# Kernel tuning notes

Hardware: AMD Instinct MI355X
Metric: run time of the kernel (lower is better)

Reference implementation:

```python
import jax, jax.numpy as jnp
import numpy as np

N = 262144  # number of points / sequence length
D = 64      # feature dim (qkv_dim); deterministic features => nb_features == D
KERNEL_EPSILON = 1e-3


def setup_inputs() -> dict:
    key = jax.random.key(0)
    ks = jax.random.split(key, 7)
    s = 1.0 / np.sqrt(D)
    return {
        "x": jax.random.normal(ks[0], (N, D), dtype=jnp.float32),
        "Wq": jax.random.normal(ks[1], (D, D), dtype=jnp.float32) * s,
        "bq": jnp.zeros((D,), dtype=jnp.float32),
        "Wk": jax.random.normal(ks[2], (D, D), dtype=jnp.float32) * s,
        "bk": jnp.zeros((D,), dtype=jnp.float32),
        "Wv": jax.random.normal(ks[3], (D, D), dtype=jnp.float32) * s,
        "bv": jnp.zeros((D,), dtype=jnp.float32),
    }


def reference(x, Wq, bq, Wk, bk, Wv, bv):
    # Dense projections (flax nn.Dense: x @ W + b)
    q = x @ Wq + bq  # [N, D]
    k = x @ Wk + bk
    v = x @ Wv + bv
    # Deterministic generalized kernel feature map: relu(data) + kernel_epsilon
    qp = jax.nn.relu(q) + KERNEL_EPSILON  # [N, M], M == D
    kp = jax.nn.relu(k) + KERNEL_EPSILON  # [N, M]
    # Bidirectional FAVOR+ linear attention: O(N*M*D)
    kv = jnp.einsum("nm,nd->md", kp, v)       # [M, D]
    num = jnp.einsum("nm,md->nd", qp, kv)     # [N, D]
    # renormalize_attention=True: divide by qp . sum(kp)
    denom = qp @ kp.sum(axis=0)               # [N]
    return num / denom[:, None]
```

## Files before the change

kernel.cpp:

```cpp
#include <hip/hip_runtime.h>
#include <hip/hip_bf16.h>


#define NPTS 262144
#define TILES (NPTS / 64)
#define GRID1 512
#define TPB1 (TILES / GRID1)
#define GRID2 1024
#define TPB2 (TILES / GRID2)
#define EPS 1e-3f

typedef __attribute__((ext_vector_type(8))) short short8;
typedef __attribute__((ext_vector_type(4))) float f32x4;

__device__ __forceinline__ unsigned short f2bf(float f) {
    unsigned u = __builtin_bit_cast(unsigned, f);
    u += 0x7FFFu + ((u >> 16) & 1u);
    return (unsigned short)(u >> 16);
}

__device__ __forceinline__ short8 load_bfrag(const float* __restrict__ W, int kk, int lg, int col) {
    short8 t;
    const float* p = W + (size_t)(kk * 32 + lg * 8) * 64 + col;
#pragma unroll
    for (int e = 0; e < 8; ++e) t[e] = (short)f2bf(p[(size_t)e * 64]);
    return t;
}

__device__ __forceinline__ short8 cvt8(float4 p0, float4 p1) {
    short8 a;
    a[0] = (short)f2bf(p0.x); a[1] = (short)f2bf(p0.y); a[2] = (short)f2bf(p0.z); a[3] = (short)f2bf(p0.w);
    a[4] = (short)f2bf(p1.x); a[5] = (short)f2bf(p1.y); a[6] = (short)f2bf(p1.z); a[7] = (short)f2bf(p1.w);
    return a;
}

__device__ __forceinline__ void lds_barrier() {
    asm volatile("s_waitcnt lgkmcnt(0)" ::: "memory");
    __builtin_amdgcn_s_barrier();
}

__global__ __launch_bounds__(256, 2) void pass1_kernel(
    const float* __restrict__ x, const float* __restrict__ Wk, const float* __restrict__ bk,
    const float* __restrict__ Wv, const float* __restrict__ bv,
    float* __restrict__ kvPart, float* __restrict__ ksPart)
{
    __shared__ unsigned short kpT[64][72];
    __shared__ unsigned short vT[64][72];
    __shared__ unsigned short wkF[8][64][8];
    __shared__ unsigned short wvF[8][64][8];

    const int tid = threadIdx.x;
    const int w = tid >> 6, l = tid & 63, l15 = l & 15, lg = l >> 4;

    {
        const float* W = (w < 2) ? Wk : Wv;
        int jbase = (w & 1) * 2;
#pragma unroll
        for (int jj = 0; jj < 2; ++jj)
#pragma unroll
            for (int kk = 0; kk < 2; ++kk) {
                short8 f = load_bfrag(W, kk, lg, (jbase + jj) * 16 + l15);
                if (w < 2) *(short8*)&wkF[(jbase + jj) * 2 + kk][l][0] = f;
                else       *(short8*)&wvF[(jbase + jj) * 2 + kk][l][0] = f;
            }
    }
    float bkl[4], bvl[4];
#pragma unroll
    for (int j = 0; j < 4; ++j) { bkl[j] = bk[j * 16 + l15]; bvl[j] = bv[j * 16 + l15]; }

    f32x4 akv[4];
#pragma unroll
    for (int j = 0; j < 4; ++j) akv[j] = (f32x4){0.f, 0.f, 0.f, 0.f};
    float ks[4] = {0.f, 0.f, 0.f, 0.f};

    lds_barrier();

    const int t0 = blockIdx.x * TPB1;
    const float* xbase = x + ((size_t)t0 * 64 + w * 16 + l15) * 64 + lg * 8;
    float4 c0 = *(const float4*)(xbase + 0);
    float4 c1 = *(const float4*)(xbase + 4);
    float4 c2 = *(const float4*)(xbase + 32);
    float4 c3 = *(const float4*)(xbase + 36);

    for (int t = 0; t < TPB1; ++t) {
        const float* xn = xbase + (size_t)((t + 1 < TPB1) ? (t + 1) : t) * 4096;
        float4 n0 = *(const float4*)(xn + 0);
        float4 n1 = *(const float4*)(xn + 4);
        float4 n2 = *(const float4*)(xn + 32);
        float4 n3 = *(const float4*)(xn + 36);

        short8 a0 = cvt8(c0, c1);
        short8 a1 = cvt8(c2, c3);

        const int nbase = w * 16 + lg * 4;
#pragma unroll
        for (int j = 0; j < 4; ++j) {
            short8 bk0 = *(const short8*)&wkF[j * 2 + 0][l][0];
            short8 bk1 = *(const short8*)&wkF[j * 2 + 1][l][0];
            short8 bv0 = *(const short8*)&wvF[j * 2 + 0][l][0];
            short8 bv1 = *(const short8*)&wvF[j * 2 + 1][l][0];
            f32x4 z = (f32x4){0.f, 0.f, 0.f, 0.f};
            f32x4 ak = __builtin_amdgcn_mfma_f32_16x16x32_bf16(a0, bk0, z, 0, 0, 0);
            ak = __builtin_amdgcn_mfma_f32_16x16x32_bf16(a1, bk1, ak, 0, 0, 0);
            f32x4 av = __builtin_amdgcn_mfma_f32_16x16x32_bf16(a0, bv0, z, 0, 0, 0);
            av = __builtin_amdgcn_mfma_f32_16x16x32_bf16(a1, bv1, av, 0, 0, 0);
            unsigned short h[4], g[4];
#pragma unroll
            for (int r = 0; r < 4; ++r) {
                float kp = fmaxf(ak[r] + bkl[j], 0.f) + EPS;
                ks[j] += kp;
                h[r] = f2bf(kp);
                g[r] = f2bf(av[r] + bvl[j]);
            }
            uint2 hp, gp;
            hp.x = (unsigned)h[0] | ((unsigned)h[1] << 16);
            hp.y = (unsigned)h[2] | ((unsigned)h[3] << 16);
            gp.x = (unsigned)g[0] | ((unsigned)g[1] << 16);
            gp.y = (unsigned)g[2] | ((unsigned)g[3] << 16);
            *(uint2*)&kpT[j * 16 + l15][nbase] = hp;
            *(uint2*)&vT[j * 16 + l15][nbase] = gp;
        }
        lds_barrier();
        short8 ka0 = *(const short8*)&kpT[w * 16 + l15][lg * 8];
        short8 ka1 = *(const short8*)&kpT[w * 16 + l15][32 + lg * 8];
#pragma unroll
        for (int j = 0; j < 4; ++j) {
            short8 vb0 = *(const short8*)&vT[j * 16 + l15][lg * 8];
            short8 vb1 = *(const short8*)&vT[j * 16 + l15][32 + lg * 8];
            akv[j] = __builtin_amdgcn_mfma_f32_16x16x32_bf16(ka0, vb0, akv[j], 0, 0, 0);
            akv[j] = __builtin_amdgcn_mfma_f32_16x16x32_bf16(ka1, vb1, akv[j], 0, 0, 0);
        }
        lds_barrier();
        c0 = n0; c1 = n1; c2 = n2; c3 = n3;
    }

    float* kvs = kvPart + (size_t)blockIdx.x * 4096;
#pragma unroll
    for (int j = 0; j < 4; ++j)
#pragma unroll
        for (int r = 0; r < 4; ++r)
            kvs[(size_t)(w * 16 + lg * 4 + r) * 64 + j * 16 + l15] = akv[j][r];
#pragma unroll
    for (int j = 0; j < 4; ++j) {
        float s = ks[j];
        s += __shfl_xor(s, 16, 64);
        s += __shfl_xor(s, 32, 64);
        if (lg == 0) ksPart[(size_t)blockIdx.x * 256 + w * 64 + j * 16 + l15] = s;
    }
}

__global__ __launch_bounds__(256, 4) void reduce_kernel(
    const float* __restrict__ kvPart, const float* __restrict__ ksPart,
    float* __restrict__ kvFin, float* __restrict__ ksFin)
{
    __shared__ float red[4][64];
    const int b = blockIdx.x, t = threadIdx.x;
    const int oo = t & 63, sc = t >> 6;
    float acc = 0.f;
    if (b < 64) {
        const float* p = kvPart + (size_t)sc * 128 * 4096 + b * 64 + oo;
#pragma unroll 8
        for (int s = 0; s < GRID1 / 4; ++s) acc += p[(size_t)s * 4096];
    } else {
        const float* p = ksPart + (size_t)sc * (GRID1) * 64 + oo;
#pragma unroll 8
        for (int s = 0; s < GRID1; ++s) acc += p[(size_t)s * 64];
    }
    red[sc][oo] = acc;
    __syncthreads();
    if (t < 64) {
        float s = red[0][t] + red[1][t] + red[2][t] + red[3][t];
        if (b < 64) kvFin[b * 64 + t] = s;
        else        ksFin[t] = s;
    }
}

__global__ __launch_bounds__(256, 4) void pass2_kernel(
    const float* __restrict__ x, const float* __restrict__ Wq, const float* __restrict__ bq,
    const float* __restrict__ kvFin, const float* __restrict__ ksFin,
    float* __restrict__ out)
{
    __shared__ unsigned short qpL[64][72];
    __shared__ unsigned short wqF[8][64][8];
    __shared__ unsigned short kvF[8][64][8];

    const int tid = threadIdx.x;
    const int w = tid >> 6, l = tid & 63, l15 = l & 15, lg = l >> 4;

#pragma unroll
    for (int kk = 0; kk < 2; ++kk) {
        short8 f = load_bfrag(Wq, kk, lg, w * 16 + l15);
        *(short8*)&wqF[w * 2 + kk][l][0] = f;
        short8 g = load_bfrag(kvFin, kk, lg, w * 16 + l15);
        *(short8*)&kvF[w * 2 + kk][l][0] = g;
    }
    float bql[4], ksl[4];
#pragma unroll
    for (int j = 0; j < 4; ++j) { bql[j] = bq[j * 16 + l15]; ksl[j] = ksFin[j * 16 + l15]; }

    lds_barrier();

    const int t0 = blockIdx.x * TPB2;
    const float* xbase = x + ((size_t)t0 * 64 + w * 16 + l15) * 64 + lg * 8;
    float4 c0 = *(const float4*)(xbase + 0);
    float4 c1 = *(const float4*)(xbase + 4);
    float4 c2 = *(const float4*)(xbase + 32);
    float4 c3 = *(const float4*)(xbase + 36);

    for (int t = 0; t < TPB2; ++t) {
        const float* xn = xbase + (size_t)((t + 1 < TPB2) ? (t + 1) : t) * 4096;
        float4 n0 = *(const float4*)(xn + 0);
        float4 n1 = *(const float4*)(xn + 4);
        float4 n2 = *(const float4*)(xn + 32);
        float4 n3 = *(const float4*)(xn + 36);

        short8 a0 = cvt8(c0, c1);
        short8 a1 = cvt8(c2, c3);

        float qp[4][4];
#pragma unroll
        for (int j = 0; j < 4; ++j) {
            short8 bq0 = *(const short8*)&wqF[j * 2 + 0][l][0];
            short8 bq1 = *(const short8*)&wqF[j * 2 + 1][l][0];
            f32x4 z = (f32x4){0.f, 0.f, 0.f, 0.f};
            f32x4 aq = __builtin_amdgcn_mfma_f32_16x16x32_bf16(a0, bq0, z, 0, 0, 0);
            aq = __builtin_amdgcn_mfma_f32_16x16x32_bf16(a1, bq1, aq, 0, 0, 0);
#pragma unroll
            for (int r = 0; r < 4; ++r) qp[j][r] = fmaxf(aq[r] + bql[j], 0.f) + EPS;
        }
        float dp[4];
#pragma unroll
        for (int r = 0; r < 4; ++r)
            dp[r] = qp[0][r] * ksl[0] + qp[1][r] * ksl[1] + qp[2][r] * ksl[2] + qp[3][r] * ksl[3];
#pragma unroll
        for (int mask = 1; mask <= 8; mask <<= 1)
#pragma unroll
            for (int r = 0; r < 4; ++r) dp[r] += __shfl_xor(dp[r], mask, 64);

        const int nb = w * 16 + lg * 4;
#pragma unroll
        for (int j = 0; j < 4; ++j)
#pragma unroll
            for (int r = 0; r < 4; ++r)
                qpL[nb + r][j * 16 + l15] = f2bf(qp[j][r]);
        lds_barrier();

        short8 an0 = *(const short8*)&qpL[w * 16 + l15][lg * 8];
        short8 an1 = *(const short8*)&qpL[w * 16 + l15][32 + lg * 8];
        float inv[4];
#pragma unroll
        for (int r = 0; r < 4; ++r) inv[r] = __builtin_amdgcn_rcpf(dp[r]);
        const int row0 = (t0 + t) * 64 + w * 16;
#pragma unroll
        for (int j = 0; j < 4; ++j) {
            short8 kv0 = *(const short8*)&kvF[j * 2 + 0][l][0];
            short8 kv1 = *(const short8*)&kvF[j * 2 + 1][l][0];
            f32x4 z = (f32x4){0.f, 0.f, 0.f, 0.f};
            f32x4 nm = __builtin_amdgcn_mfma_f32_16x16x32_bf16(an0, kv0, z, 0, 0, 0);
            nm = __builtin_amdgcn_mfma_f32_16x16x32_bf16(an1, kv1, nm, 0, 0, 0);
#pragma unroll
            for (int r = 0; r < 4; ++r)
                out[(size_t)(row0 + lg * 4 + r) * 64 + j * 16 + l15] = nm[r] * inv[r];
        }
        lds_barrier();
        c0 = n0; c1 = n1; c2 = n2; c3 = n3;
    }
}

extern "C" void kernel_launch(void* const* d_in, const int* in_sizes, int n_in,
                              void* d_out, int out_size, void* d_ws, size_t ws_size,
                              hipStream_t stream)
{
    const float* x  = (const float*)d_in[0];
    const float* Wq = (const float*)d_in[1];
    const float* bq = (const float*)d_in[2];
    const float* Wk = (const float*)d_in[3];
    const float* bk = (const float*)d_in[4];
    const float* Wv = (const float*)d_in[5];
    const float* bv = (const float*)d_in[6];
    float* out = (float*)d_out;

    float* kvPart = (float*)d_ws;
    float* ksPart = kvPart + (size_t)GRID1 * 4096;
    float* kvFin  = ksPart + (size_t)GRID1 * 256;
    float* ksFin  = kvFin + 4096;

    hipLaunchKernelGGL(pass1_kernel, dim3(GRID1), dim3(256), 0, stream,
                       x, Wk, bk, Wv, bv, kvPart, ksPart);
    hipLaunchKernelGGL(reduce_kernel, dim3(65), dim3(256), 0, stream,
                       kvPart, ksPart, kvFin, ksFin);
    hipLaunchKernelGGL(pass2_kernel, dim3(GRID2), dim3(256), 0, stream,
                       x, Wq, bq, kvFin, ksFin, out);
}
```

Baseline: 61.69 us.

## Keep KV accumulation per-wave in registers and drop block barriers in both passes

In pass1, each wave now processes two 16-row tiles at once. The K and V fragments for 32 rows are packed directly into MFMA operands, so a full 64x64 KV accumulator lives per wave in registers. This removes the per-tile LDS transpose and its two block barriers. A tree reduction through LDS at the end combines the four waves' accumulators before writing the partials. In pass2, each wave only reads back its own rows of qp, so the block barriers are replaced by a wave-local lgkmcnt drain with a double-buffered LDS tile. The cost is a 64-float accumulator array per thread in pass1, which raises register pressure and may hurt occupancy or cause spills.

```diff
diff --git a/kernel.cpp b/kernel.cpp
--- a/kernel.cpp
+++ b/kernel.cpp
@@ -6,6 +6,7 @@
 #define TILES (NPTS / 64)
 #define GRID1 512
 #define TPB1 (TILES / GRID1)
+#define PAIRS1 (TPB1 / 2)
 #define GRID2 1024
 #define TPB2 (TILES / GRID2)
 #define EPS 1e-3f
@@ -38,16 +39,19 @@
     asm volatile("s_waitcnt lgkmcnt(0)" ::: "memory");
     __builtin_amdgcn_s_barrier();
 }
+__device__ __forceinline__ void lds_drain() {
+    asm volatile("s_waitcnt lgkmcnt(0)" ::: "memory");
+}
 
 __global__ __launch_bounds__(256, 2) void pass1_kernel(
     const float* __restrict__ x, const float* __restrict__ Wk, const float* __restrict__ bk,
     const float* __restrict__ Wv, const float* __restrict__ bv,
     float* __restrict__ kvPart, float* __restrict__ ksPart)
 {
-    __shared__ unsigned short kpT[64][72];
-    __shared__ unsigned short vT[64][72];
     __shared__ unsigned short wkF[8][64][8];
     __shared__ unsigned short wvF[8][64][8];
+    __shared__ float redA[4096];
+    __shared__ float redB[4096];
 
     const int tid = threadIdx.x;
     const int w = tid >> 6, l = tid & 63, l15 = l & 15, lg = l >> 4;
@@ -68,31 +72,42 @@
 #pragma unroll
     for (int j = 0; j < 4; ++j) { bkl[j] = bk[j * 16 + l15]; bvl[j] = bv[j * 16 + l15]; }
 
-    f32x4 akv[4];
-#pragma unroll
-    for (int j = 0; j < 4; ++j) akv[j] = (f32x4){0.f, 0.f, 0.f, 0.f};
+    f32x4 akv[4][4];
+#pragma unroll
+    for (int jm = 0; jm < 4; ++jm)
+#pragma unroll
+        for (int jd = 0; jd < 4; ++jd) akv[jm][jd] = (f32x4){0.f, 0.f, 0.f, 0.f};
     float ks[4] = {0.f, 0.f, 0.f, 0.f};
 
     lds_barrier();
 
     const int t0 = blockIdx.x * TPB1;
     const float* xbase = x + ((size_t)t0 * 64 + w * 16 + l15) * 64 + lg * 8;
-    float4 c0 = *(const float4*)(xbase + 0);
-    float4 c1 = *(const float4*)(xbase + 4);
-    float4 c2 = *(const float4*)(xbase + 32);
-    float4 c3 = *(const float4*)(xbase + 36);
-
-    for (int t = 0; t < TPB1; ++t) {
-        const float* xn = xbase + (size_t)((t + 1 < TPB1) ? (t + 1) : t) * 4096;
-        float4 n0 = *(const float4*)(xn + 0);
-        float4 n1 = *(const float4*)(xn + 4);
-        float4 n2 = *(const float4*)(xn + 32);
-        float4 n3 = *(const float4*)(xn + 36);
-
-        short8 a0 = cvt8(c0, c1);
-        short8 a1 = cvt8(c2, c3);
-
-        const int nbase = w * 16 + lg * 4;
+    float4 cA0 = *(const float4*)(xbase + 0);
+    float4 cA1 = *(const float4*)(xbase + 4);
+    float4 cA2 = *(const float4*)(xbase + 32);
+    float4 cA3 = *(const float4*)(xbase + 36);
+    float4 cB0 = *(const float4*)(xbase + 4096 + 0);
+    float4 cB1 = *(const float4*)(xbase + 4096 + 4);
+    float4 cB2 = *(const float4*)(xbase + 4096 + 32);
+    float4 cB3 = *(const float4*)(xbase + 4096 + 36);
+
+#pragma unroll
+    for (int p = 0; p < PAIRS1; ++p) {
+        const float* xn = xbase + (size_t)((p + 1 < PAIRS1) ? (p + 1) : p) * 8192;
+        float4 nA0 = *(const float4*)(xn + 0);
+        float4 nA1 = *(const float4*)(xn + 4);
+        float4 nA2 = *(const float4*)(xn + 32);
+        float4 nA3 = *(const float4*)(xn + 36);
+        float4 nB0 = *(const float4*)(xn + 4096 + 0);
+        float4 nB1 = *(const float4*)(xn + 4096 + 4);
+        float4 nB2 = *(const float4*)(xn + 4096 + 32);
+        float4 nB3 = *(const float4*)(xn + 4096 + 36);
+
+        short8 a0A = cvt8(cA0, cA1), a1A = cvt8(cA2, cA3);
+        short8 a0B = cvt8(cB0, cB1), a1B = cvt8(cB2, cB3);
+
+        short8 kpc[4], vc[4];
 #pragma unroll
         for (int j = 0; j < 4; ++j) {
             short8 bk0 = *(const short8*)&wkF[j * 2 + 0][l][0];
@@ -100,46 +115,78 @@
             short8 bv0 = *(const short8*)&wvF[j * 2 + 0][l][0];
             short8 bv1 = *(const short8*)&wvF[j * 2 + 1][l][0];
             f32x4 z = (f32x4){0.f, 0.f, 0.f, 0.f};
-            f32x4 ak = __builtin_amdgcn_mfma_f32_16x16x32_bf16(a0, bk0, z, 0, 0, 0);
-            ak = __builtin_amdgcn_mfma_f32_16x16x32_bf16(a1, bk1, ak, 0, 0, 0);
-            f32x4 av = __builtin_amdgcn_mfma_f32_16x16x32_bf16(a0, bv0, z, 0, 0, 0);
-            av = __builtin_amdgcn_mfma_f32_16x16x32_bf16(a1, bv1, av, 0, 0, 0);
-            unsigned short h[4], g[4];
+            f32x4 akA = __builtin_amdgcn_mfma_f32_16x16x32_bf16(a0A, bk0, z, 0, 0, 0);
+            akA = __builtin_amdgcn_mfma_f32_16x16x32_bf16(a1A, bk1, akA, 0, 0, 0);
+            f32x4 avA = __builtin_amdgcn_mfma_f32_16x16x32_bf16(a0A, bv0, z, 0, 0, 0);
+            avA = __builtin_amdgcn_mfma_f32_16x16x32_bf16(a1A, bv1, avA, 0, 0, 0);
+            f32x4 akB = __builtin_amdgcn_mfma_f32_16x16x32_bf16(a0B, bk0, z, 0, 0, 0);
+            akB = __builtin_amdgcn_mfma_f32_16x16x32_bf16(a1B, bk1, akB, 0, 0, 0);
+            f32x4 avB = __builtin_amdgcn_mfma_f32_16x16x32_bf16(a0B, bv0, z, 0, 0, 0);
+            avB = __builtin_amdgcn_mfma_f32_16x16x32_bf16(a1B, bv1, avB, 0, 0, 0);
+            short8 kc, vv;
 #pragma unroll
             for (int r = 0; r < 4; ++r) {
-                float kp = fmaxf(ak[r] + bkl[j], 0.f) + EPS;
-                ks[j] += kp;
-                h[r] = f2bf(kp);
-                g[r] = f2bf(av[r] + bvl[j]);
+                float kA = fmaxf(akA[r] + bkl[j], 0.f) + EPS;
+                float kB = fmaxf(akB[r] + bkl[j], 0.f) + EPS;
+                ks[j] += kA + kB;
+                kc[r] = (short)f2bf(kA);
+                kc[4 + r] = (short)f2bf(kB);
+                vv[r] = (short)f2bf(avA[r] + bvl[j]);
+                vv[4 + r] = (short)f2bf(avB[r] + bvl[j]);
             }
-            uint2 hp, gp;
-            hp.x = (unsigned)h[0] | ((unsigned)h[1] << 16);
-            hp.y = (unsigned)h[2] | ((unsigned)h[3] << 16);
-            gp.x = (unsigned)g[0] | ((unsigned)g[1] << 16);
-            gp.y = (unsigned)g[2] | ((unsigned)g[3] << 16);
-            *(uint2*)&kpT[j * 16 + l15][nbase] = hp;
-            *(uint2*)&vT[j * 16 + l15][nbase] = gp;
+            kpc[j] = kc; vc[j] = vv;
         }
-        lds_barrier();
-        short8 ka0 = *(const short8*)&kpT[w * 16 + l15][lg * 8];
-        short8 ka1 = *(const short8*)&kpT[w * 16 + l15][32 + lg * 8];
-#pragma unroll
-        for (int j = 0; j < 4; ++j) {
-            short8 vb0 = *(const short8*)&vT[j * 16 + l15][lg * 8];
-            short8 vb1 = *(const short8*)&vT[j * 16 + l15][32 + lg * 8];
-            akv[j] = __builtin_amdgcn_mfma_f32_16x16x32_bf16(ka0, vb0, akv[j], 0, 0, 0);
-            akv[j] = __builtin_amdgcn_mfma_f32_16x16x32_bf16(ka1, vb1, akv[j], 0, 0, 0);
-        }
-        lds_barrier();
-        c0 = n0; c1 = n1; c2 = n2; c3 = n3;
-    }
-
-    float* kvs = kvPart + (size_t)blockIdx.x * 4096;
-#pragma unroll
-    for (int j = 0; j < 4; ++j)
-#pragma unroll
-        for (int r = 0; r < 4; ++r)
-            kvs[(size_t)(w * 16 + lg * 4 + r) * 64 + j * 16 + l15] = akv[j][r];
+#pragma unroll
+        for (int jm = 0; jm < 4; ++jm)
+#pragma unroll
+            for (int jd = 0; jd < 4; ++jd)
+                akv[jm][jd] = __builtin_amdgcn_mfma_f32_16x16x32_bf16(kpc[jm], vc[jd], akv[jm][jd], 0, 0, 0);
+
+        cA0 = nA0; cA1 = nA1; cA2 = nA2; cA3 = nA3;
+        cB0 = nB0; cB1 = nB1; cB2 = nB2; cB3 = nB3;
+    }
+
+#define KV_IDX(jm, jd, r) ((size_t)((jm) * 16 + lg * 4 + (r)) * 64 + (jd) * 16 + l15)
+    if (w == 1 || w == 3) {
+        float* dst = (w == 1) ? redA : redB;
+#pragma unroll
+        for (int jm = 0; jm < 4; ++jm)
+#pragma unroll
+            for (int jd = 0; jd < 4; ++jd)
+#pragma unroll
+                for (int r = 0; r < 4; ++r) dst[KV_IDX(jm, jd, r)] = akv[jm][jd][r];
+    }
+    __syncthreads();
+    if (w == 0 || w == 2) {
+        const float* src = (w == 0) ? redA : redB;
+#pragma unroll
+        for (int jm = 0; jm < 4; ++jm)
+#pragma unroll
+            for (int jd = 0; jd < 4; ++jd)
+#pragma unroll
+                for (int r = 0; r < 4; ++r) akv[jm][jd][r] += src[KV_IDX(jm, jd, r)];
+    }
+    __syncthreads();
+    if (w == 2) {
+#pragma unroll
+        for (int jm = 0; jm < 4; ++jm)
+#pragma unroll
+            for (int jd = 0; jd < 4; ++jd)
+#pragma unroll
+                for (int r = 0; r < 4; ++r) redA[KV_IDX(jm, jd, r)] = akv[jm][jd][r];
+    }
+    __syncthreads();
+    if (w == 0) {
+        float* kvs = kvPart + (size_t)blockIdx.x * 4096;
+#pragma unroll
+        for (int jm = 0; jm < 4; ++jm)
+#pragma unroll
+            for (int jd = 0; jd < 4; ++jd)
+#pragma unroll
+                for (int r = 0; r < 4; ++r)
+                    kvs[KV_IDX(jm, jd, r)] = akv[jm][jd][r] + redA[KV_IDX(jm, jd, r)];
+    }
+#undef KV_IDX
 #pragma unroll
     for (int j = 0; j < 4; ++j) {
         float s = ks[j];
@@ -180,7 +227,7 @@
     const float* __restrict__ kvFin, const float* __restrict__ ksFin,
     float* __restrict__ out)
 {
-    __shared__ unsigned short qpL[64][72];
+    __shared__ unsigned short qpS[2][64][72];
     __shared__ unsigned short wqF[8][64][8];
     __shared__ unsigned short kvF[8][64][8];
 
@@ -207,6 +254,7 @@
     float4 c2 = *(const float4*)(xbase + 32);
     float4 c3 = *(const float4*)(xbase + 36);
 
+#pragma unroll
     for (int t = 0; t < TPB2; ++t) {
         const float* xn = xbase + (size_t)((t + 1 < TPB2) ? (t + 1) : t) * 4096;
         float4 n0 = *(const float4*)(xn + 0);
@@ -237,16 +285,17 @@
 #pragma unroll
             for (int r = 0; r < 4; ++r) dp[r] += __shfl_xor(dp[r], mask, 64);
 
+        const int buf = t & 1;
         const int nb = w * 16 + lg * 4;
 #pragma unroll
         for (int j = 0; j < 4; ++j)
 #pragma unroll
             for (int r = 0; r < 4; ++r)
-                qpL[nb + r][j * 16 + l15] = f2bf(qp[j][r]);
-        lds_barrier();
-
-        short8 an0 = *(const short8*)&qpL[w * 16 + l15][lg * 8];
-        short8 an1 = *(const short8*)&qpL[w * 16 + l15][32 + lg * 8];
+                qpS[buf][nb + r][j * 16 + l15] = f2bf(qp[j][r]);
+        lds_drain();
+
+        short8 an0 = *(const short8*)&qpS[buf][w * 16 + l15][lg * 8];
+        short8 an1 = *(const short8*)&qpS[buf][w * 16 + l15][32 + lg * 8];
         float inv[4];
 #pragma unroll
         for (int r = 0; r < 4; ++r) inv[r] = __builtin_amdgcn_rcpf(dp[r]);
@@ -262,7 +311,6 @@
             for (int r = 0; r < 4; ++r)
                 out[(size_t)(row0 + lg * 4 + r) * 64 + j * 16 + l15] = nm[r] * inv[r];
         }
-        lds_barrier();
         c0 = n0; c1 = n1; c2 = n2; c3 = n3;
     }
 }
```

After: 67.37 us. +9.2%, slower.

## Compute Q features in pass1, store bf16 qp to workspace for pass2

Applied to the files above, without the earlier changes.

Moves the Q projection and ReLU feature map into the first pass, writing qp as bf16 to workspace so the second pass reads half-size qp instead of re-reading x in fp32 and recomputing. The denominator is computed with an MFMA against bf16-rounded key sums, and weight staging now uses coalesced row loads transposed through LDS. This trades extra workspace writes and heavier pass1 work for a lighter pass2, with roughly unchanged total DRAM bytes and slightly lower denominator precision.

```diff
diff --git a/kernel.cpp b/kernel.cpp
--- a/kernel.cpp
+++ b/kernel.cpp
@@ -19,14 +19,6 @@
     return (unsigned short)(u >> 16);
 }
 
-__device__ __forceinline__ short8 load_bfrag(const float* __restrict__ W, int kk, int lg, int col) {
-    short8 t;
-    const float* p = W + (size_t)(kk * 32 + lg * 8) * 64 + col;
-#pragma unroll
-    for (int e = 0; e < 8; ++e) t[e] = (short)f2bf(p[(size_t)e * 64]);
-    return t;
-}
-
 __device__ __forceinline__ short8 cvt8(float4 p0, float4 p1) {
     short8 a;
     a[0] = (short)f2bf(p0.x); a[1] = (short)f2bf(p0.y); a[2] = (short)f2bf(p0.z); a[3] = (short)f2bf(p0.w);
@@ -40,40 +32,66 @@
 }
 
 __global__ __launch_bounds__(256, 2) void pass1_kernel(
-    const float* __restrict__ x, const float* __restrict__ Wk, const float* __restrict__ bk,
+    const float* __restrict__ x,
+    const float* __restrict__ Wq, const float* __restrict__ bq,
+    const float* __restrict__ Wk, const float* __restrict__ bk,
     const float* __restrict__ Wv, const float* __restrict__ bv,
-    float* __restrict__ kvPart, float* __restrict__ ksPart)
+    float* __restrict__ kvPart, float* __restrict__ ksPart,
+    unsigned short* __restrict__ qpW)
 {
     __shared__ unsigned short kpT[64][72];
     __shared__ unsigned short vT[64][72];
+    __shared__ unsigned short qpT[64][72];
     __shared__ unsigned short wkF[8][64][8];
     __shared__ unsigned short wvF[8][64][8];
+    __shared__ unsigned short wqF[8][64][8];
 
     const int tid = threadIdx.x;
     const int w = tid >> 6, l = tid & 63, l15 = l & 15, lg = l >> 4;
 
     {
-        const float* W = (w < 2) ? Wk : Wv;
-        int jbase = (w & 1) * 2;
-#pragma unroll
-        for (int jj = 0; jj < 2; ++jj)
+        const float* Ws[3] = {Wk, Wv, Wq};
+        unsigned short (*Fs[3])[64][8] = {wkF, wvF, wqF};
+        const int srow = tid >> 2, sc0 = (tid & 3) * 16;
+#pragma unroll
+        for (int m = 0; m < 3; ++m) {
+            const float* p = Ws[m] + srow * 64 + sc0;
+            float4 f0 = ((const float4*)p)[0];
+            float4 f1 = ((const float4*)p)[1];
+            float4 f2 = ((const float4*)p)[2];
+            float4 f3 = ((const float4*)p)[3];
+            float ff[16] = {f0.x, f0.y, f0.z, f0.w, f1.x, f1.y, f1.z, f1.w,
+                            f2.x, f2.y, f2.z, f2.w, f3.x, f3.y, f3.z, f3.w};
+            unsigned hh[8];
+#pragma unroll
+            for (int e = 0; e < 8; ++e)
+                hh[e] = (unsigned)f2bf(ff[2 * e]) | ((unsigned)f2bf(ff[2 * e + 1]) << 16);
+            uint4 u0 = {hh[0], hh[1], hh[2], hh[3]};
+            uint4 u1 = {hh[4], hh[5], hh[6], hh[7]};
+            *(uint4*)&kpT[srow][sc0] = u0;
+            *(uint4*)&kpT[srow][sc0 + 8] = u1;
+            __syncthreads();
 #pragma unroll
             for (int kk = 0; kk < 2; ++kk) {
-                short8 f = load_bfrag(W, kk, lg, (jbase + jj) * 16 + l15);
-                if (w < 2) *(short8*)&wkF[(jbase + jj) * 2 + kk][l][0] = f;
-                else       *(short8*)&wvF[(jbase + jj) * 2 + kk][l][0] = f;
+                short8 t;
+#pragma unroll
+                for (int e = 0; e < 8; ++e)
+                    t[e] = (short)kpT[kk * 32 + lg * 8 + e][w * 16 + l15];
+                *(short8*)&Fs[m][w * 2 + kk][l][0] = t;
             }
-    }
-    float bkl[4], bvl[4];
-#pragma unroll
-    for (int j = 0; j < 4; ++j) { bkl[j] = bk[j * 16 + l15]; bvl[j] = bv[j * 16 + l15]; }
+            __syncthreads();
+        }
+    }
+    float bkl[4], bvl[4], bql[4];
+#pragma unroll
+    for (int j = 0; j < 4; ++j) {
+        bkl[j] = bk[j * 16 + l15]; bvl[j] = bv[j * 16 + l15]; bql[j] = bq[j * 16 + l15];
+    }
 
     f32x4 akv[4];
 #pragma unroll
     for (int j = 0; j < 4; ++j) akv[j] = (f32x4){0.f, 0.f, 0.f, 0.f};
     float ks[4] = {0.f, 0.f, 0.f, 0.f};
-
-    lds_barrier();
 
     const int t0 = blockIdx.x * TPB1;
     const float* xbase = x + ((size_t)t0 * 64 + w * 16 + l15) * 64 + lg * 8;
@@ -81,6 +99,7 @@
     float4 c1 = *(const float4*)(xbase + 4);
     float4 c2 = *(const float4*)(xbase + 32);
     float4 c3 = *(const float4*)(xbase + 36);
+    const int nbase = w * 16 + lg * 4;
 
     for (int t = 0; t < TPB1; ++t) {
         const float* xn = xbase + (size_t)((t + 1 < TPB1) ? (t + 1) : t) * 4096;
@@ -92,33 +111,36 @@
         short8 a0 = cvt8(c0, c1);
         short8 a1 = cvt8(c2, c3);
 
-        const int nbase = w * 16 + lg * 4;
 #pragma unroll
         for (int j = 0; j < 4; ++j) {
             short8 bk0 = *(const short8*)&wkF[j * 2 + 0][l][0];
             short8 bk1 = *(const short8*)&wkF[j * 2 + 1][l][0];
             short8 bv0 = *(const short8*)&wvF[j * 2 + 0][l][0];
             short8 bv1 = *(const short8*)&wvF[j * 2 + 1][l][0];
+            short8 bq0 = *(const short8*)&wqF[j * 2 + 0][l][0];
+            short8 bq1 = *(const short8*)&wqF[j * 2 + 1][l][0];
             f32x4 z = (f32x4){0.f, 0.f, 0.f, 0.f};
             f32x4 ak = __builtin_amdgcn_mfma_f32_16x16x32_bf16(a0, bk0, z, 0, 0, 0);
             ak = __builtin_amdgcn_mfma_f32_16x16x32_bf16(a1, bk1, ak, 0, 0, 0);
             f32x4 av = __builtin_amdgcn_mfma_f32_16x16x32_bf16(a0, bv0, z, 0, 0, 0);
             av = __builtin_amdgcn_mfma_f32_16x16x32_bf16(a1, bv1, av, 0, 0, 0);
-            unsigned short h[4], g[4];
+            f32x4 aq = __builtin_amdgcn_mfma_f32_16x16x32_bf16(a0, bq0, z, 0, 0, 0);
+            aq = __builtin_amdgcn_mfma_f32_16x16x32_bf16(a1, bq1, aq, 0, 0, 0);
+            unsigned short h[4], g[4], q[4];
 #pragma unroll
             for (int r = 0; r < 4; ++r) {
                 float kp = fmaxf(ak[r] + bkl[j], 0.f) + EPS;
                 ks[j] += kp;
                 h[r] = f2bf(kp);
                 g[r] = f2bf(av[r] + bvl[j]);
+                q[r] = f2bf(fmaxf(aq[r] + bql[j], 0.f) + EPS);
             }
-            uint2 hp, gp;
-            hp.x = (unsigned)h[0] | ((unsigned)h[1] << 16);
-            hp.y = (unsigned)h[2] | ((unsigned)h[3] << 16);
-            gp.x = (unsigned)g[0] | ((unsigned)g[1] << 16);
-            gp.y = (unsigned)g[2] | ((unsigned)g[3] << 16);
+            uint2 hp = {(unsigned)h[0] | ((unsigned)h[1] << 16), (unsigned)h[2] | ((unsigned)h[3] << 16)};
+            uint2 gp = {(unsigned)g[0] | ((unsigned)g[1] << 16), (unsigned)g[2] | ((unsigned)g[3] << 16)};
+            uint2 qp2 = {(unsigned)q[0] | ((unsigned)q[1] << 16), (unsigned)q[2] | ((unsigned)q[3] << 16)};
             *(uint2*)&kpT[j * 16 + l15][nbase] = hp;
             *(uint2*)&vT[j * 16 + l15][nbase] = gp;
+            *(uint2*)&qpT[j * 16 + l15][nbase] = qp2;
         }
         lds_barrier();
         short8 ka0 = *(const short8*)&kpT[w * 16 + l15][lg * 8];
@@ -130,6 +152,15 @@
             akv[j] = __builtin_amdgcn_mfma_f32_16x16x32_bf16(ka0, vb0, akv[j], 0, 0, 0);
             akv[j] = __builtin_amdgcn_mfma_f32_16x16x32_bf16(ka1, vb1, akv[j], 0, 0, 0);
         }
+        short8 q0, q1;
+#pragma unroll
+        for (int e = 0; e < 8; ++e) {
+            q0[e] = (short)qpT[lg * 8 + e][w * 16 + l15];
+            q1[e] = (short)qpT[32 + lg * 8 + e][w * 16 + l15];
+        }
+        unsigned short* qdst = qpW + ((size_t)(t0 + t) * 64 + w * 16 + l15) * 64 + lg * 8;
+        *(short8*)(qdst) = q0;
+        *(short8*)(qdst + 32) = q1;
         lds_barrier();
         c0 = n0; c1 = n1; c2 = n2; c3 = n3;
     }
@@ -162,7 +193,7 @@
 #pragma unroll 8
         for (int s = 0; s < GRID1 / 4; ++s) acc += p[(size_t)s * 4096];
     } else {
-        const float* p = ksPart + (size_t)sc * (GRID1) * 64 + oo;
+        const float* p = ksPart + (size_t)sc * GRID1 * 64 + oo;
 #pragma unroll 8
         for (int s = 0; s < GRID1; ++s) acc += p[(size_t)s * 64];
     }
@@ -176,94 +207,79 @@
 }
 
 __global__ __launch_bounds__(256, 4) void pass2_kernel(
-    const float* __restrict__ x, const float* __restrict__ Wq, const float* __restrict__ bq,
-    const float* __restrict__ kvFin, const float* __restrict__ ksFin,
-    float* __restrict__ out)
+    const unsigned short* __restrict__ qpW, const float* __restrict__ kvFin,
+    const float* __restrict__ ksFin, float* __restrict__ out)
 {
-    __shared__ unsigned short qpL[64][72];
-    __shared__ unsigned short wqF[8][64][8];
-    __shared__ unsigned short kvF[8][64][8];
+    __shared__ unsigned short kvS[64][72];
 
     const int tid = threadIdx.x;
     const int w = tid >> 6, l = tid & 63, l15 = l & 15, lg = l >> 4;
 
-#pragma unroll
-    for (int kk = 0; kk < 2; ++kk) {
-        short8 f = load_bfrag(Wq, kk, lg, w * 16 + l15);
-        *(short8*)&wqF[w * 2 + kk][l][0] = f;
-        short8 g = load_bfrag(kvFin, kk, lg, w * 16 + l15);
-        *(short8*)&kvF[w * 2 + kk][l][0] = g;
-    }
-    float bql[4], ksl[4];
-#pragma unroll
-    for (int j = 0; j < 4; ++j) { bql[j] = bq[j * 16 + l15]; ksl[j] = ksFin[j * 16 + l15]; }
-
-    lds_barrier();
+    {
+        const int srow = tid >> 2, sc0 = (tid & 3) * 16;
+        const float* p = kvFin + srow * 64 + sc0;
+        float4 f0 = ((const float4*)p)[0];
+        float4 f1 = ((const float4*)p)[1];
+        float4 f2 = ((const float4*)p)[2];
+        float4 f3 = ((const float4*)p)[3];
+        float ff[16] = {f0.x, f0.y, f0.z, f0.w, f1.x, f1.y, f1.z, f1.w,
+                        f2.x, f2.y, f2.z, f2.w, f3.x, f3.y, f3.z, f3.w};
+        unsigned hh[8];
+#pragma unroll
+        for (int e = 0; e < 8; ++e)
+            hh[e] = (unsigned)f2bf(ff[2 * e]) | ((unsigned)f2bf(ff[2 * e + 1]) << 16);
+        uint4 u0 = {hh[0], hh[1], hh[2], hh[3]};
+        uint4 u1 = {hh[4], hh[5], hh[6], hh[7]};
+        *(uint4*)&kvS[srow][sc0] = u0;
+        *(uint4*)&kvS[srow][sc0 + 8] = u1;
+    }
+    __syncthreads();
+    short8 kvf[4][2];
+#pragma unroll
+    for (int j = 0; j < 4; ++j)
+#pragma unroll
+        for (int kk = 0; kk < 2; ++kk) {
+            short8 t;
+#pragma unroll
+            for (int e = 0; e < 8; ++e)
+                t[e] = (short)kvS[kk * 32 + lg * 8 + e][j * 16 + l15];
+            kvf[j][kk] = t;
+        }
+    short8 ksf0, ksf1;
+#pragma unroll
+    for (int e = 0; e < 8; ++e) {
+        ksf0[e] = (short)f2bf(ksFin[lg * 8 + e]);
+        ksf1[e] = (short)f2bf(ksFin[32 + lg * 8 + e]);
+    }
 
     const int t0 = blockIdx.x * TPB2;
-    const float* xbase = x + ((size_t)t0 * 64 + w * 16 + l15) * 64 + lg * 8;
-    float4 c0 = *(const float4*)(xbase + 0);
-    float4 c1 = *(const float4*)(xbase + 4);
-    float4 c2 = *(const float4*)(xbase + 32);
-    float4 c3 = *(const float4*)(xbase + 36);
-
+    const unsigned short* qbase = qpW + ((size_t)t0 * 64 + w * 16 + l15) * 64 + lg * 8;
+    short8 an0 = *(const short8*)(qbase);
+    short8 an1 = *(const short8*)(qbase + 32);
+
+#pragma unroll
     for (int t = 0; t < TPB2; ++t) {
-        const float* xn = xbase + (size_t)((t + 1 < TPB2) ? (t + 1) : t) * 4096;
-        float4 n0 = *(const float4*)(xn + 0);
-        float4 n1 = *(const float4*)(xn + 4);
-        float4 n2 = *(const float4*)(xn + 32);
-        float4 n3 = *(const float4*)(xn + 36);
-
-        short8 a0 = cvt8(c0, c1);
-        short8 a1 = cvt8(c2, c3);
-
-        float qp[4][4];
+        const unsigned short* qn = qbase + (size_t)((t + 1 < TPB2) ? (t + 1) : t) * 4096;
+        short8 m0 = *(const short8*)(qn);
+        short8 m1 = *(const short8*)(qn + 32);
+
+        f32x4 z = (f32x4){0.f, 0.f, 0.f, 0.f};
+        f32x4 dn = __builtin_amdgcn_mfma_f32_16x16x32_bf16(an0, ksf0, z, 0, 0, 0);
+        dn = __builtin_amdgcn_mfma_f32_16x16x32_bf16(an1, ksf1, dn, 0, 0, 0);
+        float inv[4];
+#pragma unroll
+        for (int r = 0; r < 4; ++r) inv[r] = __builtin_amdgcn_rcpf(dn[r]);
+
+        const size_t row0 = (size_t)(t0 + t) * 64 + w * 16;
 #pragma unroll
         for (int j = 0; j < 4; ++j) {
-            short8 bq0 = *(const short8*)&wqF[j * 2 + 0][l][0];
-            short8 bq1 = *(const short8*)&wqF[j * 2 + 1][l][0];
-            f32x4 z = (f32x4){0.f, 0.f, 0.f, 0.f};
-            f32x4 aq = __builtin_amdgcn_mfma_f32_16x16x32_bf16(a0, bq0, z, 0, 0, 0);
-            aq = __builtin_amdgcn_mfma_f32_16x16x32_bf16(a1, bq1, aq, 0, 0, 0);
-#pragma unroll
-            for (int r = 0; r < 4; ++r) qp[j][r] = fmaxf(aq[r] + bql[j], 0.f) + EPS;
-        }
-        float dp[4];
-#pragma unroll
-        for (int r = 0; r < 4; ++r)
-            dp[r] = qp[0][r] * ksl[0] + qp[1][r] * ksl[1] + qp[2][r] * ksl[2] + qp[3][r] * ksl[3];
-#pragma unroll
-        for (int mask = 1; mask <= 8; mask <<= 1)
-#pragma unroll
-            for (int r = 0; r < 4; ++r) dp[r] += __shfl_xor(dp[r], mask, 64);
-
-        const int nb = w * 16 + lg * 4;
-#pragma unroll
-        for (int j = 0; j < 4; ++j)
+            f32x4 nm = __builtin_amdgcn_mfma_f32_16x16x32_bf16(an0, kvf[j][0], z, 0, 0, 0);
+            nm = __builtin_amdgcn_mfma_f32_16x16x32_bf16(an1, kvf[j][1], nm, 0, 0, 0);
 #pragma unroll
             for (int r = 0; r < 4; ++r)
-                qpL[nb + r][j * 16 + l15] = f2bf(qp[j][r]);
-        lds_barrier();
-
-        short8 an0 = *(const short8*)&qpL[w * 16 + l15][lg * 8];
-        short8 an1 = *(const short8*)&qpL[w * 16 + l15][32 + lg * 8];
-        float inv[4];
-#pragma unroll
-        for (int r = 0; r < 4; ++r) inv[r] = __builtin_amdgcn_rcpf(dp[r]);
-        const int row0 = (t0 + t) * 64 + w * 16;
-#pragma unroll
-        for (int j = 0; j < 4; ++j) {
-            short8 kv0 = *(const short8*)&kvF[j * 2 + 0][l][0];
-            short8 kv1 = *(const short8*)&kvF[j * 2 + 1][l][0];
-            f32x4 z = (f32x4){0.f, 0.f, 0.f, 0.f};
-            f32x4 nm = __builtin_amdgcn_mfma_f32_16x16x32_bf16(an0, kv0, z, 0, 0, 0);
-            nm = __builtin_amdgcn_mfma_f32_16x16x32_bf16(an1, kv1, nm, 0, 0, 0);
-#pragma unroll
-            for (int r = 0; r < 4; ++r)
-                out[(size_t)(row0 + lg * 4 + r) * 64 + j * 16 + l15] = nm[r] * inv[r];
-        }
-        lds_barrier();
-        c0 = n0; c1 = n1; c2 = n2; c3 = n3;
+                out[(row0 + lg * 4 + r) * 64 + j * 16 + l15] = nm[r] * inv[r];
+        }
+        an0 = m0; an1 = m1;
     }
 }
 
@@ -284,11 +300,12 @@
     float* ksPart = kvPart + (size_t)GRID1 * 4096;
     float* kvFin  = ksPart + (size_t)GRID1 * 256;
     float* ksFin  = kvFin + 4096;
+    unsigned short* qpW = (unsigned short*)(ksFin + 64);
 
     hipLaunchKernelGGL(pass1_kernel, dim3(GRID1), dim3(256), 0, stream,
-                       x, Wk, bk, Wv, bv, kvPart, ksPart);
+                       x, Wq, bq, Wk, bk, Wv, bv, kvPart, ksPart, qpW);
     hipLaunchKernelGGL(reduce_kernel, dim3(65), dim3(256), 0, stream,
                        kvPart, ksPart, kvFin, ksFin);
     hipLaunchKernelGGL(pass2_kernel, dim3(GRID2), dim3(256), 0, stream,
-                       x, Wq, bq, kvFin, ksFin, out);
-}
+                       qpW, kvFin, ksFin, out);
+}
```

Result: slower. 64.61 us (+4.7%).
